# Kernel optimization log

Measured on AMD Instinct MI355X. Metric: run time of the kernel, lower is better.

Reference implementation:

```python
import jax, jax.numpy as jnp
import numpy as np

KH, KW = 5, 5
STRIDE = 1


def _extract_patches(x, kh, kw, s):
    """x: (B,C,H,W) -> (B, oh*ow, C*kh*kw), flattened in (C,kh,kw) row-major order
    to match torch's window.reshape(B, -1)."""
    B, C, H, W = x.shape
    oh = (H - kh) // s + 1
    ow = (W - kw) // s + 1
    i = (jnp.arange(oh) * s)[:, None] + jnp.arange(kh)[None, :]      # (oh, kh)
    j = (jnp.arange(ow) * s)[:, None] + jnp.arange(kw)[None, :]      # (ow, kw)
    # fancy-index -> (B, C, oh, kh, ow, kw)
    p = x[:, :, i[:, :, None, None], j[None, None, :, :]]
    p = p.transpose(0, 2, 4, 1, 3, 5)                                # (B, oh, ow, C, kh, kw)
    return p.reshape(B, oh * ow, C * kh * kw), oh, ow


def _cdist(a, w):
    """a: (B,P,D), w: (O,D) -> Euclidean distance (B,P,O)."""
    a2 = jnp.sum(a * a, axis=-1, keepdims=True)          # (B,P,1)
    w2 = jnp.sum(w * w, axis=-1)                         # (O,)
    d2 = a2 + w2[None, None, :] - 2.0 * jnp.einsum('bpd,od->bpo', a, w)
    return jnp.sqrt(jnp.maximum(d2, 0.0))


def setup_inputs() -> dict:
    key = jax.random.key(0)
    k1, k2, k3, k4 = jax.random.split(key, 4)
    B, O = 32, 64
    H = W = 112
    gray_input = jax.random.normal(k1, (B, 1, H, W), dtype=jnp.float32)
    rgb_input = jax.random.normal(k2, (B, 1, H, W), dtype=jnp.float32)
    # kaiming-uniform-like init, first filter zeroed as in reset_parameters
    bound = 1.0 / np.sqrt(KH * KW)
    gray_weight = jax.random.uniform(k3, (O, 1, KH, KW), jnp.float32, -bound, bound)
    gray_weight = gray_weight.at[0].set(0.0)
    rgb_weight = jax.random.uniform(k4, (O, 1, KH, KW), jnp.float32, -bound, bound)
    rgb_weight = rgb_weight.at[0].set(0.0)
    std = jnp.full((1,), 2.0, dtype=jnp.float32)
    return {"gray_input": gray_input, "rgb_input": rgb_input,
            "gray_weight": gray_weight, "rgb_weight": rgb_weight, "std": std}


def reference(gray_input, rgb_input, gray_weight, rgb_weight, std):
    B = gray_input.shape[0]
    O = gray_weight.shape[0]
    gp, oh, ow = _extract_patches(gray_input, KH, KW, STRIDE)   # (B,P,D)
    rp, _, _ = _extract_patches(rgb_input, KH, KW, STRIDE)      # (B,P,D)
    gw = gray_weight.reshape(O, -1)                             # (O,D)
    rw = rgb_weight.reshape(O, -1)                              # (O,D)
    dist = _cdist(gp, gw) + _cdist(rp, rw)                      # (B,P,O)
    s = std[0]
    rbf = jnp.exp(-(dist * dist) / (2.0 * s * s))               # gaussian RBF
    return rbf.transpose(0, 2, 1).reshape(B, O, oh, ow)
```

## Files before the change

kernel.cpp:

```cpp
#include <hip/hip_runtime.h>

constexpr int KH = 5, KW = 5;
constexpr int O  = 64;
constexpr int D  = KH * KW;
constexpr int H  = 112, W = 112;
constexpr int OH = H - KH + 1;
constexpr int OW = W - KW + 1;
constexpr int P  = OH * OW;

typedef __attribute__((ext_vector_type(8))) short short8v;
typedef __attribute__((ext_vector_type(4))) float float4v;
typedef __attribute__((ext_vector_type(4))) unsigned int uint4v;

constexpr size_t WS_BYTES = 8192 * sizeof(short);

__global__ void prep_weights_mfma(const float* __restrict__ gw,
                                  const float* __restrict__ rw,
                                  void* wsv) {
    short* ws = (short*)wsv;
    const int t = threadIdx.x;
    for (int u = t; u < 512; u += 256) {
        const int lane = u & 63, mi = u >> 6;
        const int img = mi & 1, Mt = mi >> 1;
        const int hi = lane >> 4, c = lane & 15;
        const float* wt = img ? rw : gw;
        const int o = Mt * 16 + c;
        short vh[8], vl[8];
        #pragma unroll
        for (int j = 0; j < 8; ++j) {
            const int k = hi * 8 + j;
            float w;
            if (k < D) {
                w = wt[o * D + k];
            } else if (k == D) {
                float s2 = 0.f;
                for (int kk = 0; kk < D; ++kk) {
                    float x = wt[o * D + kk];
                    s2 = fmaf(x, x, s2);
                }
                w = -0.5f * s2;
            } else if (k == D + 1) {
                w = -0.5f;
            } else {
                w = 0.f;
            }
            const unsigned bits = __float_as_uint(w);
            const float hf = __uint_as_float(bits & 0xFFFF0000u);
            vh[j] = (short)(bits >> 16);
            vl[j] = (short)(__float_as_uint(w - hf) >> 16);
        }
        short* dh = ws + (mi * 64 + lane) * 8;
        short* dl = dh + 4096;
        #pragma unroll
        for (int j = 0; j < 8; ++j) { dh[j] = vh[j]; dl[j] = vl[j]; }
    }
}

__device__ inline unsigned pack_hi2(float a, float b) {
    return __builtin_amdgcn_perm(__float_as_uint(b), __float_as_uint(a),
                                 0x07060302u);
}

__global__ __launch_bounds__(256, 4) void rbf_mfma_t(
    const float* __restrict__ gin, const float* __restrict__ rin,
    const void* __restrict__ wsv,  const float* __restrict__ stdp,
    float* __restrict__ out)
{
    const short* wfrag = (const short*)wsv;
    __shared__ short wlo_s[4096];
    __shared__ float obuf[64 * 65];
    {
        const short* wlo_g = wfrag + 4096;
        for (int i = threadIdx.x; i < 512; i += 256)
            *(uint4v*)(wlo_s + i * 8) = *(const uint4v*)(wlo_g + i * 8);
    }

    const int lane = threadIdx.x & 63;
    const int hi   = lane >> 4;
    const int c    = lane & 15;
    const bool hi3 = (hi == 3);
    const int w    = threadIdx.x >> 6;
    const int q0   = blockIdx.x * 64;
    const int pw   = q0 + w * 16;

    short8v wh[8];
    #pragma unroll
    for (int mi = 0; mi < 8; ++mi)
        wh[mi] = *(const short8v*)(wfrag + (mi * 64 + lane) * 8);

    int offs[8];
    #pragma unroll
    for (int j = 0; j < 8; ++j) {
        const int k  = hi * 8 + j;
        const int ki = k / 5, kj = k - ki * 5;
        offs[j] = (k < D) ? (ki * W + kj) : 0;
    }

    const float s   = stdp[0];
    const float k2  = -1.442695040888963f / (2.f * s * s);
    const float k2a = -2.f * k2;
    const float k2b = 4.f * k2;

    __syncthreads();

    const unsigned idxp = (unsigned)(pw + c);
    const unsigned bp = idxp / (unsigned)P;
    const unsigned pp = idxp - bp * (unsigned)P;
    const unsigned yy = pp / (unsigned)OW;
    const unsigned xx = pp - yy * (unsigned)OW;
    const int ibase = (int)((bp * H + yy) * W + xx);

    short8v pfh[2], pfl[2];
    #pragma unroll
    for (int img = 0; img < 2; ++img) {
        const float* base = (img ? rin : gin) + ibase;
        float v[8];
        #pragma unroll
        for (int j = 0; j < 8; ++j) v[j] = base[offs[j]];

        float full = 0.f;
        #pragma unroll
        for (int j = 0; j < 8; ++j) full = fmaf(v[j], v[j], full);
        float part = hi3 ? v[0] * v[0] : full;
        part += __shfl_xor(part, 16);
        part += __shfl_xor(part, 32);

        float lf[8];
        #pragma unroll
        for (int j = 0; j < 8; ++j) {
            const float hf = __uint_as_float(__float_as_uint(v[j]) & 0xFFFF0000u);
            lf[j] = v[j] - hf;
        }
        uint4v uh, ul;
        uh.x = pack_hi2(v[0], v[1]);   uh.y = pack_hi2(v[2], v[3]);
        uh.z = pack_hi2(v[4], v[5]);   uh.w = pack_hi2(v[6], v[7]);
        ul.x = pack_hi2(lf[0], lf[1]); ul.y = pack_hi2(lf[2], lf[3]);
        ul.z = pack_hi2(lf[4], lf[5]); ul.w = pack_hi2(lf[6], lf[7]);

        const unsigned a2u = __float_as_uint(part);
        const float    a2t = __uint_as_float(a2u & 0xFFFF0000u);
        const unsigned aru = __float_as_uint(part - a2t);
        uh.x = hi3 ? ((uh.x & 0x0000FFFFu) | 0x3F800000u) : uh.x;
        ul.x = hi3 ? (ul.x & 0x0000FFFFu) : ul.x;
        uh.y = hi3 ? ((uh.y & 0xFFFF0000u) | (a2u >> 16)) : uh.y;
        ul.y = hi3 ? ((ul.y & 0xFFFF0000u) | (aru >> 16)) : ul.y;

        pfh[img] = __builtin_bit_cast(short8v, uh);
        pfl[img] = __builtin_bit_cast(short8v, ul);
    }

    const float4v z4 = {0.f, 0.f, 0.f, 0.f};
    #pragma unroll
    for (int Mt = 0; Mt < 4; ++Mt) {
        const short8v wlg = *(const short8v*)(wlo_s + ((Mt * 2 + 0) * 64 + lane) * 8);
        const short8v wlr = *(const short8v*)(wlo_s + ((Mt * 2 + 1) * 64 + lane) * 8);
        float4v ag4 = __builtin_amdgcn_mfma_f32_16x16x32_bf16(pfh[0], wh[Mt * 2 + 0], z4, 0, 0, 0);
        ag4 = __builtin_amdgcn_mfma_f32_16x16x32_bf16(pfh[0], wlg, ag4, 0, 0, 0);
        ag4 = __builtin_amdgcn_mfma_f32_16x16x32_bf16(pfl[0], wh[Mt * 2 + 0], ag4, 0, 0, 0);
        float4v ar4 = __builtin_amdgcn_mfma_f32_16x16x32_bf16(pfh[1], wh[Mt * 2 + 1], z4, 0, 0, 0);
        ar4 = __builtin_amdgcn_mfma_f32_16x16x32_bf16(pfh[1], wlr, ar4, 0, 0, 0);
        ar4 = __builtin_amdgcn_mfma_f32_16x16x32_bf16(pfl[1], wh[Mt * 2 + 1], ar4, 0, 0, 0);

        #pragma unroll
        for (int reg = 0; reg < 4; ++reg) {
            const float g = fminf(ag4[reg], 0.f);
            const float r = fminf(ar4[reg], 0.f);
            const float e = __builtin_amdgcn_exp2f(
                fmaf(k2a, g + r, k2b * __builtin_amdgcn_sqrtf(g * r)));
            obuf[(Mt * 16 + c) * 65 + w * 16 + hi * 4 + reg] = e;
        }
    }

    __syncthreads();

    const unsigned idxs = (unsigned)(q0 + lane);
    const unsigned bs = idxs / (unsigned)P;
    const unsigned ps = idxs - bs * (unsigned)P;
    float* obase = out + (size_t)bs * O * P + ps;
    #pragma unroll
    for (int i = 0; i < 16; ++i) {
        const int o = w * 16 + i;
        obase[(size_t)o * P] = obuf[o * 65 + lane];
    }
}

__global__ __launch_bounds__(256) void rbf_conv_fallback(
    const float* __restrict__ gin, const float* __restrict__ rin,
    const float* __restrict__ gw,  const float* __restrict__ rw,
    const float* __restrict__ stdp, float* __restrict__ out, int B)
{
    __shared__ float s_w2g[O], s_w2r[O];
    const int t = threadIdx.x;
    if (t < O) {
        float sg = 0.f, sr = 0.f;
        #pragma unroll
        for (int k = 0; k < D; ++k) {
            float a = gw[t * D + k]; sg = fmaf(a, a, sg);
            float b = rw[t * D + k]; sr = fmaf(b, b, sr);
        }
        s_w2g[t] = sg;
        s_w2r[t] = sr;
    }
    __syncthreads();

    const int idx = blockIdx.x * blockDim.x + t;
    if (idx >= B * P) return;
    const int b = idx / P;
    const int p = idx - b * P;
    const int y = p / OW;
    const int x = p - y * OW;

    const float* gb = gin + (b * H + y) * W + x;
    const float* rb = rin + (b * H + y) * W + x;
    float ga[D], ra[D];
    float a2g = 0.f, a2r = 0.f;
    #pragma unroll
    for (int i = 0; i < KH; ++i)
        #pragma unroll
        for (int j = 0; j < KW; ++j) {
            float g = gb[i * W + j]; ga[i * KW + j] = g; a2g = fmaf(g, g, a2g);
            float r = rb[i * W + j]; ra[i * KW + j] = r; a2r = fmaf(r, r, a2r);
        }

    const float s    = stdp[0];
    const float ninv = -1.0f / (2.0f * s * s);
    float* ob = out + (size_t)b * O * P + p;

    for (int o = 0; o < O; ++o) {
        float dg = 0.f, dr = 0.f;
        #pragma unroll
        for (int k = 0; k < D; ++k) {
            dg = fmaf(ga[k], gw[o * D + k], dg);
            dr = fmaf(ra[k], rw[o * D + k], dr);
        }
        float d2g = fmaxf(a2g + s_w2g[o] - 2.0f * dg, 0.f);
        float d2r = fmaxf(a2r + s_w2r[o] - 2.0f * dr, 0.f);
        float dist = __fsqrt_rn(d2g) + __fsqrt_rn(d2r);
        ob[(size_t)o * P] = __expf(ninv * dist * dist);
    }
}

extern "C" void kernel_launch(void* const* d_in, const int* in_sizes, int n_in,
                              void* d_out, int out_size, void* d_ws, size_t ws_size,
                              hipStream_t stream) {
    const float* gin  = (const float*)d_in[0];
    const float* rin  = (const float*)d_in[1];
    const float* gw   = (const float*)d_in[2];
    const float* rw   = (const float*)d_in[3];
    const float* stdp = (const float*)d_in[4];
    float* out = (float*)d_out;

    const int B  = in_sizes[0] / (H * W);
    const int BP = B * P;

    if (ws_size >= WS_BYTES && d_ws != nullptr && BP % 64 == 0) {
        prep_weights_mfma<<<1, 256, 0, stream>>>(gw, rw, d_ws);
        const int blocks = BP / 64;
        rbf_mfma_t<<<blocks, 256, 0, stream>>>(gin, rin, d_ws, stdp, out);
    } else {
        const int block = 256;
        const int grid  = (BP + block - 1) / block;
        rbf_conv_fallback<<<grid, block, 0, stream>>>(gin, rin, gw, rw, stdp, out, B);
    }
}
```

Before: 34.53 us.

## Enlarge MFMA RBF blocks to 256 pixels with vectorized float4 output stores

Blocks now use 512 threads and cover 256 output pixels, with each wave handling two 16-pixel groups whose input loads are all issued before compute. The shared output tile is widened (stride 264), so each thread writes contiguous float4 chunks per output channel instead of scalar stores. A slow scalar path handles blocks that straddle an image boundary. The goals are wider coalesced stores, more memory-level parallelism, and amortized weight staging, at the cost of much more shared memory per block (about 75 KB) and lower occupancy.

```diff
diff --git a/kernel.cpp b/kernel.cpp
--- a/kernel.cpp
+++ b/kernel.cpp
@@ -7,6 +7,8 @@
 constexpr int OH = H - KH + 1;
 constexpr int OW = W - KW + 1;
 constexpr int P  = OH * OW;
+constexpr int BLK_PX = 256;
+constexpr int OSTRIDE = 264;
 
 typedef __attribute__((ext_vector_type(8))) short short8v;
 typedef __attribute__((ext_vector_type(4))) float float4v;
@@ -61,27 +63,30 @@
                                  0x07060302u);
 }
 
-__global__ __launch_bounds__(256, 4) void rbf_mfma_t(
+__global__ __launch_bounds__(512, 4) void rbf_mfma_t(
     const float* __restrict__ gin, const float* __restrict__ rin,
     const void* __restrict__ wsv,  const float* __restrict__ stdp,
     float* __restrict__ out)
 {
     const short* wfrag = (const short*)wsv;
     __shared__ short wlo_s[4096];
-    __shared__ float obuf[64 * 65];
+    __shared__ float obuf[64 * OSTRIDE];
     {
         const short* wlo_g = wfrag + 4096;
-        for (int i = threadIdx.x; i < 512; i += 256)
-            *(uint4v*)(wlo_s + i * 8) = *(const uint4v*)(wlo_g + i * 8);
-    }
+        for (int i = threadIdx.x; i < 512; i += 512)
+            ;
+        for (int i = threadIdx.x; i < 512; i += 512)
+            ;
+    }
+    for (int i = threadIdx.x; i < 512; i += 512)
+        *(uint4v*)(wlo_s + i * 8) = *(const uint4v*)((const short*)wfrag + 4096 + i * 8);
 
     const int lane = threadIdx.x & 63;
     const int hi   = lane >> 4;
     const int c    = lane & 15;
     const bool hi3 = (hi == 3);
     const int w    = threadIdx.x >> 6;
-    const int q0   = blockIdx.x * 64;
-    const int pw   = q0 + w * 16;
+    const int q0   = blockIdx.x * BLK_PX;
 
     short8v wh[8];
     #pragma unroll
@@ -103,84 +108,115 @@
 
     __syncthreads();
 
-    const unsigned idxp = (unsigned)(pw + c);
-    const unsigned bp = idxp / (unsigned)P;
-    const unsigned pp = idxp - bp * (unsigned)P;
-    const unsigned yy = pp / (unsigned)OW;
-    const unsigned xx = pp - yy * (unsigned)OW;
-    const int ibase = (int)((bp * H + yy) * W + xx);
-
-    short8v pfh[2], pfl[2];
-    #pragma unroll
-    for (int img = 0; img < 2; ++img) {
-        const float* base = (img ? rin : gin) + ibase;
-        float v[8];
+    auto ibase_of = [&](int pxbase) -> int {
+        const unsigned idxp = (unsigned)(q0 + pxbase + c);
+        const unsigned bp = idxp / (unsigned)P;
+        const unsigned pp = idxp - bp * (unsigned)P;
+        const unsigned yy = pp / (unsigned)OW;
+        const unsigned xx = pp - yy * (unsigned)OW;
+        return (int)((bp * H + yy) * W + xx);
+    };
+
+    auto load8 = [&](float (&v)[8], const float* base) {
         #pragma unroll
         for (int j = 0; j < 8; ++j) v[j] = base[offs[j]];
-
-        float full = 0.f;
-        #pragma unroll
-        for (int j = 0; j < 8; ++j) full = fmaf(v[j], v[j], full);
-        float part = hi3 ? v[0] * v[0] : full;
-        part += __shfl_xor(part, 16);
-        part += __shfl_xor(part, 32);
-
-        float lf[8];
-        #pragma unroll
-        for (int j = 0; j < 8; ++j) {
-            const float hf = __uint_as_float(__float_as_uint(v[j]) & 0xFFFF0000u);
-            lf[j] = v[j] - hf;
-        }
-        uint4v uh, ul;
-        uh.x = pack_hi2(v[0], v[1]);   uh.y = pack_hi2(v[2], v[3]);
-        uh.z = pack_hi2(v[4], v[5]);   uh.w = pack_hi2(v[6], v[7]);
-        ul.x = pack_hi2(lf[0], lf[1]); ul.y = pack_hi2(lf[2], lf[3]);
-        ul.z = pack_hi2(lf[4], lf[5]); ul.w = pack_hi2(lf[6], lf[7]);
-
-        const unsigned a2u = __float_as_uint(part);
-        const float    a2t = __uint_as_float(a2u & 0xFFFF0000u);
-        const unsigned aru = __float_as_uint(part - a2t);
-        uh.x = hi3 ? ((uh.x & 0x0000FFFFu) | 0x3F800000u) : uh.x;
-        ul.x = hi3 ? (ul.x & 0x0000FFFFu) : ul.x;
-        uh.y = hi3 ? ((uh.y & 0xFFFF0000u) | (a2u >> 16)) : uh.y;
-        ul.y = hi3 ? ((ul.y & 0xFFFF0000u) | (aru >> 16)) : ul.y;
-
-        pfh[img] = __builtin_bit_cast(short8v, uh);
-        pfl[img] = __builtin_bit_cast(short8v, ul);
-    }
-
-    const float4v z4 = {0.f, 0.f, 0.f, 0.f};
-    #pragma unroll
-    for (int Mt = 0; Mt < 4; ++Mt) {
-        const short8v wlg = *(const short8v*)(wlo_s + ((Mt * 2 + 0) * 64 + lane) * 8);
-        const short8v wlr = *(const short8v*)(wlo_s + ((Mt * 2 + 1) * 64 + lane) * 8);
-        float4v ag4 = __builtin_amdgcn_mfma_f32_16x16x32_bf16(pfh[0], wh[Mt * 2 + 0], z4, 0, 0, 0);
-        ag4 = __builtin_amdgcn_mfma_f32_16x16x32_bf16(pfh[0], wlg, ag4, 0, 0, 0);
-        ag4 = __builtin_amdgcn_mfma_f32_16x16x32_bf16(pfl[0], wh[Mt * 2 + 0], ag4, 0, 0, 0);
-        float4v ar4 = __builtin_amdgcn_mfma_f32_16x16x32_bf16(pfh[1], wh[Mt * 2 + 1], z4, 0, 0, 0);
-        ar4 = __builtin_amdgcn_mfma_f32_16x16x32_bf16(pfh[1], wlr, ar4, 0, 0, 0);
-        ar4 = __builtin_amdgcn_mfma_f32_16x16x32_bf16(pfl[1], wh[Mt * 2 + 1], ar4, 0, 0, 0);
-
-        #pragma unroll
-        for (int reg = 0; reg < 4; ++reg) {
-            const float g = fminf(ag4[reg], 0.f);
-            const float r = fminf(ar4[reg], 0.f);
-            const float e = __builtin_amdgcn_exp2f(
-                fmaf(k2a, g + r, k2b * __builtin_amdgcn_sqrtf(g * r)));
-            obuf[(Mt * 16 + c) * 65 + w * 16 + hi * 4 + reg] = e;
-        }
-    }
+    };
+
+    auto process = [&](const float (&vg)[8], const float (&vr)[8], int pxbase) {
+        short8v pfh[2], pfl[2];
+        #pragma unroll
+        for (int img = 0; img < 2; ++img) {
+            const float (&v)[8] = img ? vr : vg;
+            float full = 0.f;
+            #pragma unroll
+            for (int j = 0; j < 8; ++j) full = fmaf(v[j], v[j], full);
+            float part = hi3 ? v[0] * v[0] : full;
+            part += __shfl_xor(part, 16);
+            part += __shfl_xor(part, 32);
+
+            float lf[8];
+            #pragma unroll
+            for (int j = 0; j < 8; ++j) {
+                const float hf = __uint_as_float(__float_as_uint(v[j]) & 0xFFFF0000u);
+                lf[j] = v[j] - hf;
+            }
+            uint4v uh, ul;
+            uh.x = pack_hi2(v[0], v[1]);   uh.y = pack_hi2(v[2], v[3]);
+            uh.z = pack_hi2(v[4], v[5]);   uh.w = pack_hi2(v[6], v[7]);
+            ul.x = pack_hi2(lf[0], lf[1]); ul.y = pack_hi2(lf[2], lf[3]);
+            ul.z = pack_hi2(lf[4], lf[5]); ul.w = pack_hi2(lf[6], lf[7]);
+
+            const unsigned a2u = __float_as_uint(part);
+            const float    a2t = __uint_as_float(a2u & 0xFFFF0000u);
+            const unsigned aru = __float_as_uint(part - a2t);
+            uh.x = hi3 ? ((uh.x & 0x0000FFFFu) | 0x3F800000u) : uh.x;
+            ul.x = hi3 ? (ul.x & 0x0000FFFFu) : ul.x;
+            uh.y = hi3 ? ((uh.y & 0xFFFF0000u) | (a2u >> 16)) : uh.y;
+            ul.y = hi3 ? ((ul.y & 0xFFFF0000u) | (aru >> 16)) : ul.y;
+
+            pfh[img] = __builtin_bit_cast(short8v, uh);
+            pfl[img] = __builtin_bit_cast(short8v, ul);
+        }
+
+        const float4v z4 = {0.f, 0.f, 0.f, 0.f};
+        #pragma unroll
+        for (int Mt = 0; Mt < 4; ++Mt) {
+            const short8v wlg = *(const short8v*)(wlo_s + ((Mt * 2 + 0) * 64 + lane) * 8);
+            const short8v wlr = *(const short8v*)(wlo_s + ((Mt * 2 + 1) * 64 + lane) * 8);
+            float4v ag4 = __builtin_amdgcn_mfma_f32_16x16x32_bf16(pfh[0], wh[Mt * 2 + 0], z4, 0, 0, 0);
+            ag4 = __builtin_amdgcn_mfma_f32_16x16x32_bf16(pfh[0], wlg, ag4, 0, 0, 0);
+            ag4 = __builtin_amdgcn_mfma_f32_16x16x32_bf16(pfl[0], wh[Mt * 2 + 0], ag4, 0, 0, 0);
+            float4v ar4 = __builtin_amdgcn_mfma_f32_16x16x32_bf16(pfh[1], wh[Mt * 2 + 1], z4, 0, 0, 0);
+            ar4 = __builtin_amdgcn_mfma_f32_16x16x32_bf16(pfh[1], wlr, ar4, 0, 0, 0);
+            ar4 = __builtin_amdgcn_mfma_f32_16x16x32_bf16(pfl[1], wh[Mt * 2 + 1], ar4, 0, 0, 0);
+
+            #pragma unroll
+            for (int reg = 0; reg < 4; ++reg) {
+                const float g = fminf(ag4[reg], 0.f);
+                const float r = fminf(ar4[reg], 0.f);
+                const float e = __builtin_amdgcn_exp2f(
+                    fmaf(k2a, g + r, k2b * __builtin_amdgcn_sqrtf(g * r)));
+                obuf[(Mt * 16 + c) * OSTRIDE + pxbase + hi * 4 + reg] = e;
+            }
+        }
+    };
+
+    const int px0 = w * 16;
+    const int px1 = 128 + w * 16;
+    const int ib0 = ibase_of(px0);
+    const int ib1 = ibase_of(px1);
+    float v0g[8], v0r[8], v1g[8], v1r[8];
+    load8(v0g, gin + ib0); load8(v0r, rin + ib0);
+    load8(v1g, gin + ib1); load8(v1r, rin + ib1);
+    process(v0g, v0r, px0);
+    process(v1g, v1r, px1);
 
     __syncthreads();
 
-    const unsigned idxs = (unsigned)(q0 + lane);
-    const unsigned bs = idxs / (unsigned)P;
-    const unsigned ps = idxs - bs * (unsigned)P;
-    float* obase = out + (size_t)bs * O * P + ps;
-    #pragma unroll
-    for (int i = 0; i < 16; ++i) {
-        const int o = w * 16 + i;
-        obase[(size_t)o * P] = obuf[o * 65 + lane];
+    const int q0m = q0 % P;
+    const bool straddle = (q0m + BLK_PX > P);
+    if (!straddle) {
+        const int bs = q0 / P;
+        float* obase = out + (size_t)bs * O * P + q0m;
+        #pragma unroll
+        for (int i = 0; i < 8; ++i) {
+            const int o = w * 8 + i;
+            const float4v vv = *(const float4v*)(&obuf[o * OSTRIDE + 4 * lane]);
+            *(float4v*)(obase + (size_t)o * P + 4 * lane) = vv;
+        }
+    } else {
+        #pragma unroll
+        for (int i = 0; i < 8; ++i) {
+            const int o = w * 8 + i;
+            #pragma unroll
+            for (int jj = 0; jj < 4; ++jj) {
+                const int px = 4 * lane + jj;
+                const unsigned idxs = (unsigned)(q0 + px);
+                const unsigned bs = idxs / (unsigned)P;
+                const unsigned ps = idxs - bs * (unsigned)P;
+                out[(size_t)bs * O * P + (size_t)o * P + ps] = obuf[o * OSTRIDE + px];
+            }
+        }
     }
 }
 
@@ -253,10 +289,10 @@
     const int B  = in_sizes[0] / (H * W);
     const int BP = B * P;
 
-    if (ws_size >= WS_BYTES && d_ws != nullptr && BP % 64 == 0) {
+    if (ws_size >= WS_BYTES && d_ws != nullptr && BP % BLK_PX == 0) {
         prep_weights_mfma<<<1, 256, 0, stream>>>(gw, rw, d_ws);
-        const int blocks = BP / 64;
-        rbf_mfma_t<<<blocks, 256, 0, stream>>>(gin, rin, d_ws, stdp, out);
+        const int blocks = BP / BLK_PX;
+        rbf_mfma_t<<<blocks, 512, 0, stream>>>(gin, rin, d_ws, stdp, out);
     } else {
         const int block = 256;
         const int grid  = (BP + block - 1) / block;
```

New measurement: 39.87 us. 15.5% more time.

## Process two pixel tiles per block with float2 nontemporal output stores

Applied to the files above, without the earlier changes.

Each block now covers 128 output pixels instead of 64. Each wave loads both of its 16-pixel input tiles before running the MFMA work, which spreads the per-block weight staging over more work and keeps more global loads in flight. The LDS output buffer is widened with an odd row stride, and the write-back uses float2 nontemporal stores so each lane writes two adjacent pixels. Launch bounds drop to 3 blocks per SM to make room for the larger shared buffer and register use. The risks are lower occupancy and float2 LDS reads that are not 8-byte aligned on odd rows because the stride is odd.

```diff
diff --git a/kernel.cpp b/kernel.cpp
--- a/kernel.cpp
+++ b/kernel.cpp
@@ -7,9 +7,12 @@
 constexpr int OH = H - KH + 1;
 constexpr int OW = W - KW + 1;
 constexpr int P  = OH * OW;
+constexpr int BLK_PX = 128;
+constexpr int OSTR   = 133;
 
 typedef __attribute__((ext_vector_type(8))) short short8v;
 typedef __attribute__((ext_vector_type(4))) float float4v;
+typedef __attribute__((ext_vector_type(2))) float float2v;
 typedef __attribute__((ext_vector_type(4))) unsigned int uint4v;
 
 constexpr size_t WS_BYTES = 8192 * sizeof(short);
@@ -61,14 +64,14 @@
                                  0x07060302u);
 }
 
-__global__ __launch_bounds__(256, 4) void rbf_mfma_t(
+__global__ __launch_bounds__(256, 3) void rbf_mfma_t(
     const float* __restrict__ gin, const float* __restrict__ rin,
     const void* __restrict__ wsv,  const float* __restrict__ stdp,
     float* __restrict__ out)
 {
     const short* wfrag = (const short*)wsv;
     __shared__ short wlo_s[4096];
-    __shared__ float obuf[64 * 65];
+    __shared__ float obuf[64 * OSTR];
     {
         const short* wlo_g = wfrag + 4096;
         for (int i = threadIdx.x; i < 512; i += 256)
@@ -80,8 +83,7 @@
     const int c    = lane & 15;
     const bool hi3 = (hi == 3);
     const int w    = threadIdx.x >> 6;
-    const int q0   = blockIdx.x * 64;
-    const int pw   = q0 + w * 16;
+    const int q0   = blockIdx.x * BLK_PX;
 
     short8v wh[8];
     #pragma unroll
@@ -103,84 +105,95 @@
 
     __syncthreads();
 
-    const unsigned idxp = (unsigned)(pw + c);
-    const unsigned bp = idxp / (unsigned)P;
-    const unsigned pp = idxp - bp * (unsigned)P;
-    const unsigned yy = pp / (unsigned)OW;
-    const unsigned xx = pp - yy * (unsigned)OW;
-    const int ibase = (int)((bp * H + yy) * W + xx);
-
-    short8v pfh[2], pfl[2];
-    #pragma unroll
-    for (int img = 0; img < 2; ++img) {
-        const float* base = (img ? rin : gin) + ibase;
-        float v[8];
-        #pragma unroll
-        for (int j = 0; j < 8; ++j) v[j] = base[offs[j]];
-
-        float full = 0.f;
-        #pragma unroll
-        for (int j = 0; j < 8; ++j) full = fmaf(v[j], v[j], full);
-        float part = hi3 ? v[0] * v[0] : full;
-        part += __shfl_xor(part, 16);
-        part += __shfl_xor(part, 32);
-
-        float lf[8];
-        #pragma unroll
-        for (int j = 0; j < 8; ++j) {
-            const float hf = __uint_as_float(__float_as_uint(v[j]) & 0xFFFF0000u);
-            lf[j] = v[j] - hf;
-        }
-        uint4v uh, ul;
-        uh.x = pack_hi2(v[0], v[1]);   uh.y = pack_hi2(v[2], v[3]);
-        uh.z = pack_hi2(v[4], v[5]);   uh.w = pack_hi2(v[6], v[7]);
-        ul.x = pack_hi2(lf[0], lf[1]); ul.y = pack_hi2(lf[2], lf[3]);
-        ul.z = pack_hi2(lf[4], lf[5]); ul.w = pack_hi2(lf[6], lf[7]);
-
-        const unsigned a2u = __float_as_uint(part);
-        const float    a2t = __uint_as_float(a2u & 0xFFFF0000u);
-        const unsigned aru = __float_as_uint(part - a2t);
-        uh.x = hi3 ? ((uh.x & 0x0000FFFFu) | 0x3F800000u) : uh.x;
-        ul.x = hi3 ? (ul.x & 0x0000FFFFu) : ul.x;
-        uh.y = hi3 ? ((uh.y & 0xFFFF0000u) | (a2u >> 16)) : uh.y;
-        ul.y = hi3 ? ((ul.y & 0xFFFF0000u) | (aru >> 16)) : ul.y;
-
-        pfh[img] = __builtin_bit_cast(short8v, uh);
-        pfl[img] = __builtin_bit_cast(short8v, ul);
-    }
-
-    const float4v z4 = {0.f, 0.f, 0.f, 0.f};
-    #pragma unroll
-    for (int Mt = 0; Mt < 4; ++Mt) {
-        const short8v wlg = *(const short8v*)(wlo_s + ((Mt * 2 + 0) * 64 + lane) * 8);
-        const short8v wlr = *(const short8v*)(wlo_s + ((Mt * 2 + 1) * 64 + lane) * 8);
-        float4v ag4 = __builtin_amdgcn_mfma_f32_16x16x32_bf16(pfh[0], wh[Mt * 2 + 0], z4, 0, 0, 0);
-        ag4 = __builtin_amdgcn_mfma_f32_16x16x32_bf16(pfh[0], wlg, ag4, 0, 0, 0);
-        ag4 = __builtin_amdgcn_mfma_f32_16x16x32_bf16(pfl[0], wh[Mt * 2 + 0], ag4, 0, 0, 0);
-        float4v ar4 = __builtin_amdgcn_mfma_f32_16x16x32_bf16(pfh[1], wh[Mt * 2 + 1], z4, 0, 0, 0);
-        ar4 = __builtin_amdgcn_mfma_f32_16x16x32_bf16(pfh[1], wlr, ar4, 0, 0, 0);
-        ar4 = __builtin_amdgcn_mfma_f32_16x16x32_bf16(pfl[1], wh[Mt * 2 + 1], ar4, 0, 0, 0);
-
-        #pragma unroll
-        for (int reg = 0; reg < 4; ++reg) {
-            const float g = fminf(ag4[reg], 0.f);
-            const float r = fminf(ar4[reg], 0.f);
-            const float e = __builtin_amdgcn_exp2f(
-                fmaf(k2a, g + r, k2b * __builtin_amdgcn_sqrtf(g * r)));
-            obuf[(Mt * 16 + c) * 65 + w * 16 + hi * 4 + reg] = e;
-        }
-    }
+    auto loadTile = [&](int tOff, float (&vg)[8], float (&vr)[8]) {
+        const unsigned idxp = (unsigned)(q0 + tOff + c);
+        const unsigned bp = idxp / (unsigned)P;
+        const unsigned pp = idxp - bp * (unsigned)P;
+        const unsigned yy = pp / (unsigned)OW;
+        const unsigned xx = pp - yy * (unsigned)OW;
+        const int ibase = (int)((bp * H + yy) * W + xx);
+        #pragma unroll
+        for (int j = 0; j < 8; ++j) vg[j] = gin[ibase + offs[j]];
+        #pragma unroll
+        for (int j = 0; j < 8; ++j) vr[j] = rin[ibase + offs[j]];
+    };
+
+    auto processTile = [&](const float (&vgt)[8], const float (&vrt)[8], int tOff) {
+        short8v pfh[2], pfl[2];
+        #pragma unroll
+        for (int img = 0; img < 2; ++img) {
+            const float (&v)[8] = img ? vrt : vgt;
+            float full = 0.f;
+            #pragma unroll
+            for (int j = 0; j < 8; ++j) full = fmaf(v[j], v[j], full);
+            float part = hi3 ? v[0] * v[0] : full;
+            part += __shfl_xor(part, 16);
+            part += __shfl_xor(part, 32);
+
+            float lf[8];
+            #pragma unroll
+            for (int j = 0; j < 8; ++j) {
+                const float hf = __uint_as_float(__float_as_uint(v[j]) & 0xFFFF0000u);
+                lf[j] = v[j] - hf;
+            }
+            uint4v uh, ul;
+            uh.x = pack_hi2(v[0], v[1]);   uh.y = pack_hi2(v[2], v[3]);
+            uh.z = pack_hi2(v[4], v[5]);   uh.w = pack_hi2(v[6], v[7]);
+            ul.x = pack_hi2(lf[0], lf[1]); ul.y = pack_hi2(lf[2], lf[3]);
+            ul.z = pack_hi2(lf[4], lf[5]); ul.w = pack_hi2(lf[6], lf[7]);
+
+            const unsigned a2u = __float_as_uint(part);
+            const float    a2t = __uint_as_float(a2u & 0xFFFF0000u);
+            const unsigned aru = __float_as_uint(part - a2t);
+            uh.x = hi3 ? ((uh.x & 0x0000FFFFu) | 0x3F800000u) : uh.x;
+            ul.x = hi3 ? (ul.x & 0x0000FFFFu) : ul.x;
+            uh.y = hi3 ? ((uh.y & 0xFFFF0000u) | (a2u >> 16)) : uh.y;
+            ul.y = hi3 ? ((ul.y & 0xFFFF0000u) | (aru >> 16)) : ul.y;
+
+            pfh[img] = __builtin_bit_cast(short8v, uh);
+            pfl[img] = __builtin_bit_cast(short8v, ul);
+        }
+
+        const float4v z4 = {0.f, 0.f, 0.f, 0.f};
+        #pragma unroll
+        for (int Mt = 0; Mt < 4; ++Mt) {
+            const short8v wlg = *(const short8v*)(wlo_s + ((Mt * 2 + 0) * 64 + lane) * 8);
+            const short8v wlr = *(const short8v*)(wlo_s + ((Mt * 2 + 1) * 64 + lane) * 8);
+            float4v ag4 = __builtin_amdgcn_mfma_f32_16x16x32_bf16(pfh[0], wh[Mt * 2 + 0], z4, 0, 0, 0);
+            ag4 = __builtin_amdgcn_mfma_f32_16x16x32_bf16(pfh[0], wlg, ag4, 0, 0, 0);
+            ag4 = __builtin_amdgcn_mfma_f32_16x16x32_bf16(pfl[0], wh[Mt * 2 + 0], ag4, 0, 0, 0);
+            float4v ar4 = __builtin_amdgcn_mfma_f32_16x16x32_bf16(pfh[1], wh[Mt * 2 + 1], z4, 0, 0, 0);
+            ar4 = __builtin_amdgcn_mfma_f32_16x16x32_bf16(pfh[1], wlr, ar4, 0, 0, 0);
+            ar4 = __builtin_amdgcn_mfma_f32_16x16x32_bf16(pfl[1], wh[Mt * 2 + 1], ar4, 0, 0, 0);
+
+            #pragma unroll
+            for (int reg = 0; reg < 4; ++reg) {
+                const float g = fminf(ag4[reg], 0.f);
+                const float r = fminf(ar4[reg], 0.f);
+                const float e = __builtin_amdgcn_exp2f(
+                    fmaf(k2a, g + r, k2b * __builtin_amdgcn_sqrtf(g * r)));
+                obuf[(Mt * 16 + c) * OSTR + tOff + hi * 4 + reg] = e;
+            }
+        }
+    };
+
+    float vAg[8], vAr[8], vBg[8], vBr[8];
+    loadTile(w * 16, vAg, vAr);
+    loadTile(64 + w * 16, vBg, vBr);
+    processTile(vAg, vAr, w * 16);
+    processTile(vBg, vBr, 64 + w * 16);
 
     __syncthreads();
 
-    const unsigned idxs = (unsigned)(q0 + lane);
+    const unsigned idxs = (unsigned)(q0 + 2 * lane);
     const unsigned bs = idxs / (unsigned)P;
     const unsigned ps = idxs - bs * (unsigned)P;
     float* obase = out + (size_t)bs * O * P + ps;
     #pragma unroll
     for (int i = 0; i < 16; ++i) {
         const int o = w * 16 + i;
-        obase[(size_t)o * P] = obuf[o * 65 + lane];
+        const float2v vv = *(const float2v*)(&obuf[o * OSTR + 2 * lane]);
+        __builtin_nontemporal_store(vv, (float2v*)(obase + (size_t)o * P));
     }
 }
 
@@ -253,9 +266,9 @@
     const int B  = in_sizes[0] / (H * W);
     const int BP = B * P;
 
-    if (ws_size >= WS_BYTES && d_ws != nullptr && BP % 64 == 0) {
+    if (ws_size >= WS_BYTES && d_ws != nullptr && BP % BLK_PX == 0) {
         prep_weights_mfma<<<1, 256, 0, stream>>>(gw, rw, d_ws);
-        const int blocks = BP / 64;
+        const int blocks = BP / BLK_PX;
         rbf_mfma_t<<<blocks, 256, 0, stream>>>(gin, rin, d_ws, stdp, out);
     } else {
         const int block = 256;
```

Result: no change. 33.97 us (-1.6%).
